# Performance work log

Hardware: AMD Instinct MI355X
Metric: run time of the kernel (lower is better)

Reference implementation:

```python
import jax, jax.numpy as jnp
import numpy as np

N_TOKENS = 100000
N_ARGS = 20000
N_EDGES = 320000
IN_DIM = 768
HEADS = 8
OUT_DIM = 64


def setup_inputs() -> dict:
    key = jax.random.key(0)
    k1, k2, k3, k4, k5 = jax.random.split(key, 5)
    h = jax.random.normal(k1, (N_TOKENS, IN_DIM), dtype=jnp.float32)
    W_fc = jax.random.normal(k2, (HEADS * OUT_DIM, IN_DIM), dtype=jnp.float32) * 0.05
    a_attn = jax.random.normal(k3, (2 * OUT_DIM,), dtype=jnp.float32) * 0.1
    edge_src = jax.random.randint(k4, (N_EDGES,), 0, N_TOKENS, dtype=jnp.int32)
    edge_dst = jax.random.randint(k5, (N_EDGES,), 0, N_ARGS, dtype=jnp.int32)
    return {"h": h, "W_fc": W_fc, "a_attn": a_attn,
            "edge_src": edge_src, "edge_dst": edge_dst}


def reference(h, W_fc, a_attn, edge_src, edge_dst):
    # z = fc(h) reshaped to [N_TOKENS, HEADS, OUT_DIM]
    z = (h @ W_fc.T).reshape(N_TOKENS, HEADS, OUT_DIM)
    # DGL zero-initializes 'z' on arg (dst) nodes, so the dst half of attn_fc
    # contributes 0; only the src half of the attention vector matters.
    a_src = a_attn[:OUT_DIM]
    s_node = jnp.einsum('nhd,d->nh', z, a_src)            # [N_TOKENS, H]
    e = jax.nn.leaky_relu(s_node[edge_src])               # [E, H]
    # segment softmax over incoming edges of each arg node
    m = jax.ops.segment_max(e, edge_dst, num_segments=N_ARGS)   # [N_ARGS, H]
    ex = jnp.exp(e - m[edge_dst])                          # [E, H]
    denom = jax.ops.segment_sum(ex, edge_dst, num_segments=N_ARGS)
    denom = jnp.where(denom == 0, 1.0, denom)
    alpha = ex / denom[edge_dst]                           # [E, H]
    # weighted neighbor aggregation
    msg = alpha[:, :, None] * z[edge_src]                  # [E, H, D]
    out = jax.ops.segment_sum(msg, edge_dst, num_segments=N_ARGS)  # [N_ARGS, H, D]
    return out
```

## Files before the change

kernel.cpp:

```cpp
#include <hip/hip_runtime.h>
#include <hip/hip_bf16.h>
#include <stdint.h>

#define N_TOKENS 100000
#define N_ARGS   20000
#define N_EDGES  320000
#define IN_DIM   768
#define HEADS    8
#define OUT_DIM  64
#define ZDIM     512

typedef unsigned short u16;
typedef unsigned int   u32;
typedef __bf16 bf16x8 __attribute__((ext_vector_type(8)));
typedef float  f32x4  __attribute__((ext_vector_type(4)));

__device__ __forceinline__ u16 f2bf(float f) {
    union { float f; u32 i; } v; v.f = f;
    u32 u = v.i;
    u += 0x7fffu + ((u >> 16) & 1u);
    return (u16)(u >> 16);
}
__device__ __forceinline__ float bf2f(u16 u) {
    union { u32 i; float f; } v; v.i = ((u32)u) << 16; return v.f;
}
__device__ __forceinline__ u32 pk(float lo, float hi) {
    __hip_bfloat162 r = __float22bfloat162_rn(float2{lo, hi});
    union { __hip_bfloat162 b; u32 u; } v; v.b = r; return v.u;
}
__device__ __forceinline__ uint4 pack8(const float4 p, const float4 q) {
    uint4 w;
    w.x = pk(p.x, p.y); w.y = pk(p.z, p.w);
    w.z = pk(q.x, q.y); w.w = pk(q.z, q.w);
    return w;
}
__device__ __forceinline__ void load_lds16(const void* g, void* l) {
    __builtin_amdgcn_global_load_lds(
        (const __attribute__((address_space(1))) void*)g,
        (__attribute__((address_space(3))) void*)l, 16, 0, 0);
}

__global__ __launch_bounds__(256) void convert_w(const float* __restrict__ W,
                                                 u16* __restrict__ Wbf) {
    const int i = blockIdx.x * blockDim.x + threadIdx.x;
    if (i < ZDIM * IN_DIM / 8) {
        const float4* p = reinterpret_cast<const float4*>(W + (size_t)i * 8);
        const float4 x = p[0], y = p[1];
        reinterpret_cast<uint4*>(Wbf)[i] = pack8(x, y);
    }
}

__global__ __launch_bounds__(256) void gemm_kernel(
    const float* __restrict__ A,
    const u16*   __restrict__ Bbf,
    const float* __restrict__ a_attn,
    u16* __restrict__ z,
    float* __restrict__ s_node)
{
    __shared__ float As[2][128 * 32];
    __shared__ u16   Bs[2][128 * 32];

    const int tid  = threadIdx.x;
    const int wave = tid >> 6, lane = tid & 63;
    const int quad = lane >> 4, l16 = lane & 15;
    const int wm = wave >> 1, wn = wave & 1;

    const int bx = blockIdx.x;
    const int lb = (bx & 7) * 391 + (bx >> 3);
    const int tileN = lb & 3;
    const int tileM = lb >> 2;

    const char* srcA[4];
    int         dA[4];
#pragma unroll
    for (int g = 0; g < 4; g++) {
        const int idx = (wave * 4 + g) * 64 + lane;
        const int row = idx >> 3, s = idx & 7;
        const int c = s ^ (row & 7);
        int grow = tileM * 128 + row;
        if (grow >= N_TOKENS) grow = N_TOKENS - 1;
        srcA[g] = (const char*)(A + (size_t)grow * IN_DIM + c * 4);
        dA[g] = (wave * 4 + g) * 1024;
    }
    const char* srcB[2];
    int         dB[2];
#pragma unroll
    for (int g = 0; g < 2; g++) {
        const int idx = (wave * 2 + g) * 64 + lane;
        const int row = idx >> 2, s = idx & 3;
        const int c = s ^ ((row >> 1) & 3);
        srcB[g] = (const char*)(Bbf + (size_t)(tileN * 128 + row) * IN_DIM + c * 8);
        dB[g] = (wave * 2 + g) * 1024;
    }

    const char* rA0[4];
    const char* rA1[4];
    const char* rB[4];
#pragma unroll
    for (int i = 0; i < 4; i++) {
        int r = wm * 64 + i * 16 + l16;
        const int sl = (quad * 2) ^ (r & 7);
        rA0[i] = (const char*)As + r * 128 + sl * 16;
        rA1[i] = (const char*)As + r * 128 + (sl ^ 1) * 16;
        r = wn * 64 + i * 16 + l16;
        rB[i] = (const char*)Bs + r * 64 + ((quad ^ ((r >> 1) & 3)) * 16);
    }

    f32x4 acc[4][4];
    const f32x4 zero4 = {0.f, 0.f, 0.f, 0.f};
#pragma unroll
    for (int i = 0; i < 4; i++)
#pragma unroll
        for (int j = 0; j < 4; j++) acc[i][j] = zero4;

#pragma unroll
    for (int g = 0; g < 4; g++) load_lds16(srcA[g], (char*)As + dA[g]);
#pragma unroll
    for (int g = 0; g < 2; g++) load_lds16(srcB[g], (char*)Bs + dB[g]);
    __syncthreads();

    for (int kt = 0; kt < IN_DIM / 32; ++kt) {
        const int cur = kt & 1;
        const int nxt = cur ^ 1;

        if (kt < IN_DIM / 32 - 1) {
#pragma unroll
            for (int g = 0; g < 4; g++)
                load_lds16(srcA[g] + (size_t)(kt + 1) * 128,
                           (char*)As + nxt * 16384 + dA[g]);
#pragma unroll
            for (int g = 0; g < 2; g++)
                load_lds16(srcB[g] + (size_t)(kt + 1) * 64,
                           (char*)Bs + nxt * 8192 + dB[g]);
        }

        bf16x8 aF[4], bF[4];
#pragma unroll
        for (int i = 0; i < 4; i++) {
            const float4 lo = *reinterpret_cast<const float4*>(rA0[i] + cur * 16384);
            const float4 hi = *reinterpret_cast<const float4*>(rA1[i] + cur * 16384);
            union { uint4 u; bf16x8 b; } cv;
            cv.u = pack8(lo, hi);
            aF[i] = cv.b;
        }
#pragma unroll
        for (int j = 0; j < 4; j++)
            bF[j] = *reinterpret_cast<const bf16x8*>(rB[j] + cur * 8192);
#pragma unroll
        for (int i = 0; i < 4; i++)
#pragma unroll
            for (int j = 0; j < 4; j++)
                acc[i][j] = __builtin_amdgcn_mfma_f32_16x16x32_bf16(aF[i], bF[j], acc[i][j], 0, 0, 0);

        __syncthreads();
    }

    float av[4];
#pragma unroll
    for (int j = 0; j < 4; j++) av[j] = a_attn[j * 16 + l16];
    const int head = tileN * 2 + wn;
    const int colb = tileN * 128 + wn * 64;
#pragma unroll
    for (int i = 0; i < 4; i++) {
        const int rowb = tileM * 128 + wm * 64 + i * 16 + quad * 4;
#pragma unroll
        for (int r = 0; r < 4; r++) {
            const int row = rowb + r;
            const bool ok = row < N_TOKENS;
            float p = 0.0f;
#pragma unroll
            for (int j = 0; j < 4; j++) {
                const float v = acc[i][j][r];
                p += v * av[j];
                if (ok) z[(size_t)row * ZDIM + colb + j * 16 + l16] = f2bf(v);
            }
            p += __shfl_xor(p, 1);
            p += __shfl_xor(p, 2);
            p += __shfl_xor(p, 4);
            p += __shfl_xor(p, 8);
            if (ok && l16 == 0) s_node[row * HEADS + head] = p;
        }
    }
}

__global__ void zero_kernel(int* __restrict__ p, int n) {
    int i = blockIdx.x * blockDim.x + threadIdx.x;
    if (i < n) p[i] = 0;
}

__global__ void hist_kernel(const int* __restrict__ edst, int* __restrict__ counts) {
    int i = blockIdx.x * blockDim.x + threadIdx.x;
    if (i < N_EDGES) {
        int d = edst[i];
        if ((unsigned)d < (unsigned)N_ARGS) atomicAdd(&counts[d], 1);
    }
}

__global__ void scan_kernel(const int* __restrict__ counts, int* __restrict__ offsets,
                            int* __restrict__ cursor) {
    __shared__ int partial[1024];
    const int tid = threadIdx.x;
    const int C = 20;
    const int base = tid * C;
    int s = 0;
    for (int k = 0; k < C; k++) { int idx = base + k; if (idx < N_ARGS) s += counts[idx]; }
    partial[tid] = s;
    __syncthreads();
    for (int off = 1; off < 1024; off <<= 1) {
        int v = (tid >= off) ? partial[tid - off] : 0;
        __syncthreads();
        partial[tid] += v;
        __syncthreads();
    }
    int run = (tid == 0) ? 0 : partial[tid - 1];
    for (int k = 0; k < C; k++) {
        int idx = base + k;
        if (idx < N_ARGS) { offsets[idx] = run; cursor[idx] = run; run += counts[idx]; }
    }
    if (tid == 1023) offsets[N_ARGS] = run;
}

__global__ void scatter_kernel(const int* __restrict__ esrc, const int* __restrict__ edst,
                               int* __restrict__ cursor, int* __restrict__ ssrc) {
    int i = blockIdx.x * blockDim.x + threadIdx.x;
    if (i < N_EDGES) {
        int d = edst[i];
        if ((unsigned)d >= (unsigned)N_ARGS) return;
        int s = esrc[i];
        if ((unsigned)s >= (unsigned)N_TOKENS) s = 0;
        int pos = atomicAdd(&cursor[d], 1);
        ssrc[pos] = s;
    }
}

__global__ __launch_bounds__(256) void agg_kernel(
    const int* __restrict__ offsets, const int* __restrict__ sorted_src,
    const float* __restrict__ s_node, const u16* __restrict__ z,
    float* __restrict__ out)
{
    const int tid  = threadIdx.x;
    const int wave = tid >> 6, lane = tid & 63;
    const int dst  = blockIdx.x * 4 + wave;

    __shared__ int   src_s[4][64];
    __shared__ float alpha_s[4][512];

    if (dst >= N_ARGS) return;

    const int start = offsets[dst];
    const int nE = offsets[dst + 1] - start;
    float* op = out + (size_t)dst * ZDIM + lane * 8;
    if (nE <= 0) {
        const f32x4 zz = {0.f, 0.f, 0.f, 0.f};
        *reinterpret_cast<f32x4*>(op)     = zz;
        *reinterpret_cast<f32x4*>(op + 4) = zz;
        return;
    }
    int*   srcw = src_s[wave];
    float* alw  = alpha_s[wave];
    const int hsel = lane >> 3;

    float m[8], ssum[8];
#pragma unroll
    for (int h = 0; h < 8; h++) { m[h] = -1e30f; ssum[h] = 0.f; }

    for (int c0 = 0; c0 < nE; c0 += 64) {
        float v[8];
        const bool act = (c0 + lane) < nE;
        if (act) {
            int s = sorted_src[start + c0 + lane];
            if ((unsigned)s >= (unsigned)N_TOKENS) s = 0;
            const float4* p = reinterpret_cast<const float4*>(s_node + (size_t)s * 8);
            const float4 x = p[0], y = p[1];
            v[0]=x.x; v[1]=x.y; v[2]=x.z; v[3]=x.w;
            v[4]=y.x; v[5]=y.y; v[6]=y.z; v[7]=y.w;
#pragma unroll
            for (int h = 0; h < 8; h++) v[h] = v[h] > 0.f ? v[h] : 0.01f * v[h];
        } else {
#pragma unroll
            for (int h = 0; h < 8; h++) v[h] = -1e30f;
        }
        float cm[8];
#pragma unroll
        for (int h = 0; h < 8; h++) cm[h] = v[h];
#pragma unroll
        for (int off = 1; off < 64; off <<= 1)
#pragma unroll
            for (int h = 0; h < 8; h++) cm[h] = fmaxf(cm[h], __shfl_xor(cm[h], off));
        float ce[8];
#pragma unroll
        for (int h = 0; h < 8; h++) {
            const float mn = fmaxf(m[h], cm[h]);
            ce[h] = act ? __expf(v[h] - mn) : 0.f;
            ssum[h] *= __expf(m[h] - mn);
            m[h] = mn;
        }
#pragma unroll
        for (int off = 1; off < 64; off <<= 1)
#pragma unroll
            for (int h = 0; h < 8; h++) ce[h] += __shfl_xor(ce[h], off);
#pragma unroll
        for (int h = 0; h < 8; h++) ssum[h] += ce[h];
    }
    float inv[8];
#pragma unroll
    for (int h = 0; h < 8; h++) {
        float d = ssum[h]; if (d == 0.f) d = 1.f; inv[h] = 1.f / d;
    }

    f32x4 acc0 = {0.f,0.f,0.f,0.f}, acc1 = {0.f,0.f,0.f,0.f};
    for (int c0 = 0; c0 < nE; c0 += 64) {
        const int cn = min(64, nE - c0);
        if (lane < cn) {
            int s = sorted_src[start + c0 + lane];
            if ((unsigned)s >= (unsigned)N_TOKENS) s = 0;
            srcw[lane] = s;
            const float4* p = reinterpret_cast<const float4*>(s_node + (size_t)s * 8);
            const float4 x = p[0], y = p[1];
            float v[8];
            v[0]=x.x; v[1]=x.y; v[2]=x.z; v[3]=x.w;
            v[4]=y.x; v[5]=y.y; v[6]=y.z; v[7]=y.w;
#pragma unroll
            for (int h = 0; h < 8; h++) {
                const float u = v[h] > 0.f ? v[h] : 0.01f * v[h];
                alw[lane * 8 + h] = __expf(u - m[h]) * inv[h];
            }
        }
        asm volatile("s_waitcnt lgkmcnt(0)" ::: "memory");
        for (int j = 0; j < cn; ++j) {
            const int   row = srcw[j];
            const float a   = alw[j * 8 + hsel];
            const uint4 zr  = *reinterpret_cast<const uint4*>(
                                  z + (size_t)row * ZDIM + lane * 8);
            acc0.x += a * bf2f((u16)(zr.x & 0xffffu));
            acc0.y += a * bf2f((u16)(zr.x >> 16));
            acc0.z += a * bf2f((u16)(zr.y & 0xffffu));
            acc0.w += a * bf2f((u16)(zr.y >> 16));
            acc1.x += a * bf2f((u16)(zr.z & 0xffffu));
            acc1.y += a * bf2f((u16)(zr.z >> 16));
            acc1.z += a * bf2f((u16)(zr.w & 0xffffu));
            acc1.w += a * bf2f((u16)(zr.w >> 16));
        }
    }
    *reinterpret_cast<f32x4*>(op)     = acc0;
    *reinterpret_cast<f32x4*>(op + 4) = acc1;
}

extern "C" void kernel_launch(void* const* d_in, const int* in_sizes, int n_in,
                              void* d_out, int out_size, void* d_ws, size_t ws_size,
                              hipStream_t stream) {
    const float* h      = (const float*)d_in[0];
    const float* W      = (const float*)d_in[1];
    const float* a_attn = (const float*)d_in[2];
    const int* esrc     = (const int*)d_in[3];
    const int* edst     = (const int*)d_in[4];
    float* out          = (float*)d_out;

    char* ws = (char*)d_ws;
    u16*   z        = (u16*)ws;
    float* s_node   = (float*)(ws + 102400000);
    int*   counts   = (int*)(ws + 105600000);
    int*   offsets  = (int*)(ws + 105680000);
    int*   cursor   = (int*)(ws + 105760016);
    int*   ssrc     = (int*)(ws + 105840016);
    u16*   wbf      = (u16*)(ws + 107120016);

    zero_kernel<<<(N_ARGS + 255) / 256, 256, 0, stream>>>(counts, N_ARGS);
    convert_w<<<(ZDIM * IN_DIM / 8 + 255) / 256, 256, 0, stream>>>(W, wbf);
    gemm_kernel<<<782 * 4, 256, 0, stream>>>(h, wbf, a_attn, z, s_node);
    hist_kernel<<<(N_EDGES + 255) / 256, 256, 0, stream>>>(edst, counts);
    scan_kernel<<<1, 1024, 0, stream>>>(counts, offsets, cursor);
    scatter_kernel<<<(N_EDGES + 255) / 256, 256, 0, stream>>>(esrc, edst, cursor, ssrc);
    agg_kernel<<<(N_ARGS + 3) / 4, 256, 0, stream>>>(offsets, ssrc, s_node, z, out);
}
```

Measured before the change: 711.9 us.

## Widen GEMM tile to 128x256, single-buffer LDS, and stage scan counts in LDS

```diff
diff --git a/kernel.cpp b/kernel.cpp
--- a/kernel.cpp
+++ b/kernel.cpp
@@ -57,8 +57,8 @@
     u16* __restrict__ z,
     float* __restrict__ s_node)
 {
-    __shared__ float As[2][128 * 32];
-    __shared__ u16   Bs[2][128 * 32];
+    __shared__ float As[128 * 32];
+    __shared__ u16   Bs[256 * 32];
 
     const int tid  = threadIdx.x;
     const int wave = tid >> 6, lane = tid & 63;
@@ -66,9 +66,10 @@
     const int wm = wave >> 1, wn = wave & 1;
 
     const int bx = blockIdx.x;
-    const int lb = (bx & 7) * 391 + (bx >> 3);
-    const int tileN = lb & 3;
-    const int tileM = lb >> 2;
+    const int lb = (bx & 7) * 196 + (bx >> 3);
+    if (lb >= 782 * 2) return;
+    const int tileN2 = lb & 1;
+    const int tileM  = lb >> 1;
 
     const char* srcA[4];
     int         dA[4];
@@ -82,84 +83,82 @@
         srcA[g] = (const char*)(A + (size_t)grow * IN_DIM + c * 4);
         dA[g] = (wave * 4 + g) * 1024;
     }
-    const char* srcB[2];
-    int         dB[2];
-#pragma unroll
-    for (int g = 0; g < 2; g++) {
-        const int idx = (wave * 2 + g) * 64 + lane;
+    const char* srcB[4];
+    int         dB[4];
+#pragma unroll
+    for (int g = 0; g < 4; g++) {
+        const int idx = (wave * 4 + g) * 64 + lane;
         const int row = idx >> 2, s = idx & 3;
         const int c = s ^ ((row >> 1) & 3);
-        srcB[g] = (const char*)(Bbf + (size_t)(tileN * 128 + row) * IN_DIM + c * 8);
-        dB[g] = (wave * 2 + g) * 1024;
-    }
-
-    const char* rA0[4];
-    const char* rA1[4];
-    const char* rB[4];
+        srcB[g] = (const char*)(Bbf + (size_t)(tileN2 * 256 + row) * IN_DIM + c * 8);
+        dB[g] = (wave * 4 + g) * 1024;
+    }
+
+    const float* rA0[4];
+    const float* rA1[4];
+    const u16*   rB[8];
 #pragma unroll
     for (int i = 0; i < 4; i++) {
-        int r = wm * 64 + i * 16 + l16;
+        const int r = wm * 64 + i * 16 + l16;
         const int sl = (quad * 2) ^ (r & 7);
-        rA0[i] = (const char*)As + r * 128 + sl * 16;
-        rA1[i] = (const char*)As + r * 128 + (sl ^ 1) * 16;
-        r = wn * 64 + i * 16 + l16;
-        rB[i] = (const char*)Bs + r * 64 + ((quad ^ ((r >> 1) & 3)) * 16);
-    }
-
-    f32x4 acc[4][4];
+        rA0[i] = As + r * 32 + sl * 4;
+        rA1[i] = As + r * 32 + (sl ^ 1) * 4;
+    }
+#pragma unroll
+    for (int j = 0; j < 8; j++) {
+        const int r = wn * 128 + j * 16 + l16;
+        rB[j] = Bs + r * 32 + ((quad ^ ((r >> 1) & 3)) * 8);
+    }
+
+    f32x4 acc[4][8];
     const f32x4 zero4 = {0.f, 0.f, 0.f, 0.f};
 #pragma unroll
     for (int i = 0; i < 4; i++)
 #pragma unroll
-        for (int j = 0; j < 4; j++) acc[i][j] = zero4;
-
-#pragma unroll
-    for (int g = 0; g < 4; g++) load_lds16(srcA[g], (char*)As + dA[g]);
-#pragma unroll
-    for (int g = 0; g < 2; g++) load_lds16(srcB[g], (char*)Bs + dB[g]);
-    __syncthreads();
+        for (int j = 0; j < 8; j++) acc[i][j] = zero4;
 
     for (int kt = 0; kt < IN_DIM / 32; ++kt) {
-        const int cur = kt & 1;
-        const int nxt = cur ^ 1;
-
-        if (kt < IN_DIM / 32 - 1) {
-#pragma unroll
-            for (int g = 0; g < 4; g++)
-                load_lds16(srcA[g] + (size_t)(kt + 1) * 128,
-                           (char*)As + nxt * 16384 + dA[g]);
-#pragma unroll
-            for (int g = 0; g < 2; g++)
-                load_lds16(srcB[g] + (size_t)(kt + 1) * 64,
-                           (char*)Bs + nxt * 8192 + dB[g]);
-        }
-
-        bf16x8 aF[4], bF[4];
+        __syncthreads();
+#pragma unroll
+        for (int g = 0; g < 4; g++) load_lds16(srcA[g], (char*)As + dA[g]);
+#pragma unroll
+        for (int g = 0; g < 4; g++) load_lds16(srcB[g], (char*)Bs + dB[g]);
+        __syncthreads();
+
+        bf16x8 aF[4];
 #pragma unroll
         for (int i = 0; i < 4; i++) {
-            const float4 lo = *reinterpret_cast<const float4*>(rA0[i] + cur * 16384);
-            const float4 hi = *reinterpret_cast<const float4*>(rA1[i] + cur * 16384);
+            const float4 lo = *reinterpret_cast<const float4*>(rA0[i]);
+            const float4 hi = *reinterpret_cast<const float4*>(rA1[i]);
             union { uint4 u; bf16x8 b; } cv;
             cv.u = pack8(lo, hi);
             aF[i] = cv.b;
         }
 #pragma unroll
-        for (int j = 0; j < 4; j++)
-            bF[j] = *reinterpret_cast<const bf16x8*>(rB[j] + cur * 8192);
-#pragma unroll
-        for (int i = 0; i < 4; i++)
+        for (int jj = 0; jj < 2; jj++) {
+            bf16x8 bF[4];
 #pragma unroll
             for (int j = 0; j < 4; j++)
-                acc[i][j] = __builtin_amdgcn_mfma_f32_16x16x32_bf16(aF[i], bF[j], acc[i][j], 0, 0, 0);
-
-        __syncthreads();
+                bF[j] = *reinterpret_cast<const bf16x8*>(rB[jj * 4 + j]);
+#pragma unroll
+            for (int i = 0; i < 4; i++)
+#pragma unroll
+                for (int j = 0; j < 4; j++)
+                    acc[i][jj * 4 + j] = __builtin_amdgcn_mfma_f32_16x16x32_bf16(
+                        aF[i], bF[j], acc[i][jj * 4 + j], 0, 0, 0);
+        }
+
+#pragma unroll
+        for (int g = 0; g < 4; g++) srcA[g] += 128;
+#pragma unroll
+        for (int g = 0; g < 4; g++) srcB[g] += 64;
     }
 
     float av[4];
 #pragma unroll
     for (int j = 0; j < 4; j++) av[j] = a_attn[j * 16 + l16];
-    const int head = tileN * 2 + wn;
-    const int colb = tileN * 128 + wn * 64;
+    const int hb   = tileN2 * 4 + wn * 2;
+    const int colb = tileN2 * 256 + wn * 128;
 #pragma unroll
     for (int i = 0; i < 4; i++) {
         const int rowb = tileM * 128 + wm * 64 + i * 16 + quad * 4;
@@ -167,18 +166,27 @@
         for (int r = 0; r < 4; r++) {
             const int row = rowb + r;
             const bool ok = row < N_TOKENS;
-            float p = 0.0f;
+            float p0 = 0.0f, p1 = 0.0f;
 #pragma unroll
             for (int j = 0; j < 4; j++) {
                 const float v = acc[i][j][r];
-                p += v * av[j];
+                p0 += v * av[j];
                 if (ok) z[(size_t)row * ZDIM + colb + j * 16 + l16] = f2bf(v);
             }
-            p += __shfl_xor(p, 1);
-            p += __shfl_xor(p, 2);
-            p += __shfl_xor(p, 4);
-            p += __shfl_xor(p, 8);
-            if (ok && l16 == 0) s_node[row * HEADS + head] = p;
+#pragma unroll
+            for (int j = 0; j < 4; j++) {
+                const float v = acc[i][4 + j][r];
+                p1 += v * av[j];
+                if (ok) z[(size_t)row * ZDIM + colb + 64 + j * 16 + l16] = f2bf(v);
+            }
+            p0 += __shfl_xor(p0, 1); p1 += __shfl_xor(p1, 1);
+            p0 += __shfl_xor(p0, 2); p1 += __shfl_xor(p1, 2);
+            p0 += __shfl_xor(p0, 4); p1 += __shfl_xor(p1, 4);
+            p0 += __shfl_xor(p0, 8); p1 += __shfl_xor(p1, 8);
+            if (ok && l16 == 0) {
+                s_node[row * HEADS + hb]     = p0;
+                s_node[row * HEADS + hb + 1] = p1;
+            }
         }
     }
 }
@@ -198,12 +206,16 @@
 
 __global__ void scan_kernel(const int* __restrict__ counts, int* __restrict__ offsets,
                             int* __restrict__ cursor) {
+    __shared__ int cbuf[N_ARGS];
     __shared__ int partial[1024];
     const int tid = threadIdx.x;
+    for (int i = tid; i < N_ARGS; i += 1024) cbuf[i] = counts[i];
+    __syncthreads();
     const int C = 20;
     const int base = tid * C;
     int s = 0;
-    for (int k = 0; k < C; k++) { int idx = base + k; if (idx < N_ARGS) s += counts[idx]; }
+#pragma unroll
+    for (int k = 0; k < C; k++) { int idx = base + k; if (idx < N_ARGS) s += cbuf[idx]; }
     partial[tid] = s;
     __syncthreads();
     for (int off = 1; off < 1024; off <<= 1) {
@@ -212,12 +224,20 @@
         partial[tid] += v;
         __syncthreads();
     }
+    const int total = partial[1023];
     int run = (tid == 0) ? 0 : partial[tid - 1];
+#pragma unroll
     for (int k = 0; k < C; k++) {
         int idx = base + k;
-        if (idx < N_ARGS) { offsets[idx] = run; cursor[idx] = run; run += counts[idx]; }
-    }
-    if (tid == 1023) offsets[N_ARGS] = run;
+        if (idx < N_ARGS) { int c = cbuf[idx]; cbuf[idx] = run; run += c; }
+    }
+    __syncthreads();
+    for (int i = tid; i < N_ARGS; i += 1024) {
+        const int v = cbuf[i];
+        offsets[i] = v;
+        cursor[i]  = v;
+    }
+    if (tid == 1023) offsets[N_ARGS] = total;
 }
 
 __global__ void scatter_kernel(const int* __restrict__ esrc, const int* __restrict__ edst,
@@ -367,7 +387,7 @@
 
     zero_kernel<<<(N_ARGS + 255) / 256, 256, 0, stream>>>(counts, N_ARGS);
     convert_w<<<(ZDIM * IN_DIM / 8 + 255) / 256, 256, 0, stream>>>(W, wbf);
-    gemm_kernel<<<782 * 4, 256, 0, stream>>>(h, wbf, a_attn, z, s_node);
+    gemm_kernel<<<1568, 256, 0, stream>>>(h, wbf, a_attn, z, s_node);
     hist_kernel<<<(N_EDGES + 255) / 256, 256, 0, stream>>>(edst, counts);
     scan_kernel<<<1, 1024, 0, stream>>>(counts, offsets, cursor);
     scatter_kernel<<<(N_EDGES + 255) / 256, 256, 0, stream>>>(esrc, edst, cursor, ssrc);
```

Measured after the change: 747.7 us. 5.0% more time.
